# Optimization experiments

Hardware: AMD Instinct MI355X
Metric: run time of the kernel (lower is better)

## Reference

```python
import jax, jax.numpy as jnp
import numpy as np

N = 50000
D = 128
E = 600000


def setup_inputs() -> dict:
    key = jax.random.key(0)
    k1, k2, k3, k4, k5, k6 = jax.random.split(key, 6)
    x = jax.random.normal(k1, (N, D), dtype=jnp.float32)
    edge_index = jax.random.randint(k2, (2, E), 0, N, dtype=jnp.int32)
    s = 1.0 / np.sqrt(D)
    W1 = jax.random.uniform(k3, (D, D), dtype=jnp.float32, minval=-s, maxval=s)
    b1 = jax.random.uniform(k4, (D,), dtype=jnp.float32, minval=-s, maxval=s)
    W2 = jax.random.uniform(k5, (D, D), dtype=jnp.float32, minval=-s, maxval=s)
    b2 = jax.random.uniform(k6, (D,), dtype=jnp.float32, minval=-s, maxval=s)
    return {"x": x, "edge_index": edge_index, "W1": W1, "b1": b1, "W2": W2, "b2": b2}


def _gcn_conv(x, src, dst, W, b):
    # PyG GCNConv (default flow source->target): out[dst] += norm * (x @ W)[src] + b
    n = x.shape[0]
    deg = jax.ops.segment_sum(jnp.ones_like(dst, dtype=x.dtype), dst, num_segments=n)
    dinv = jnp.where(deg > 0, jax.lax.rsqrt(deg), 0.0)
    norm = dinv[src] * dinv[dst]          # [E+N]
    h = x @ W                             # [N, D]
    msg = h[src] * norm[:, None]          # [E+N, D] gather + scale
    out = jax.ops.segment_sum(msg, dst, num_segments=n)
    return out + b


def reference(x, edge_index, W1, b1, W2, b2):
    n = x.shape[0]
    loops = jnp.arange(n, dtype=edge_index.dtype)
    src = jnp.concatenate([edge_index[0], loops])  # add self-loops
    dst = jnp.concatenate([edge_index[1], loops])
    h = jax.nn.relu(_gcn_conv(x, src, dst, W1, b1))
    out = jax.nn.relu(_gcn_conv(h, src, dst, W2, b2))
    return out
```

## Files before the change

### kernel.cpp

```cpp
#include <hip/hip_runtime.h>
#include <stdint.h>

typedef __attribute__((ext_vector_type(8))) short bf16x8;
typedef __attribute__((ext_vector_type(4))) float f32x4;

#define CAP 64
#define SEGCAP 4096

__device__ __forceinline__ float bf2f(unsigned int u) {
    union { unsigned int i; float f; } v; v.i = u << 16; return v.f;
}
__device__ __forceinline__ unsigned int f2bf(float f) {
    union { float f; unsigned int i; } v; v.f = f;
    unsigned int b = v.i;
    b += 0x7FFFu + ((b >> 16) & 1u);
    return b >> 16;
}


__global__ __launch_bounds__(256) void partition_kernel(
    const int* __restrict__ src, const int* __restrict__ dst, int E,
    unsigned int* __restrict__ gcnt,
    unsigned int* __restrict__ seg,
    const float* __restrict__ W1, const float* __restrict__ W2,
    unsigned short* __restrict__ Wt1, unsigned short* __restrict__ Wt2)
{
    __shared__ unsigned int hist[256];
    int tid = threadIdx.x;
    int t = blockIdx.x * 256 + tid;

    if (t < 32768) {
        const float* W = (t < 16384) ? W1 : W2;
        unsigned short* O = (t < 16384) ? Wt1 : Wt2;
        int i = t & 16383;
        O[i] = (unsigned short)f2bf(W[(i & 127) * 128 + (i >> 7)]);
    }

    hist[tid] = 0;
    __syncthreads();

    int e0 = blockIdx.x * 2048 + tid * 8;
    unsigned int pair[8]; int rng[8]; bool val[8];
    if (e0 + 8 <= E) {
        int4 a0 = *(const int4*)(src + e0), a1 = *(const int4*)(src + e0 + 4);
        int4 b0 = *(const int4*)(dst + e0), b1 = *(const int4*)(dst + e0 + 4);
        int sa[8] = {a0.x,a0.y,a0.z,a0.w,a1.x,a1.y,a1.z,a1.w};
        int da[8] = {b0.x,b0.y,b0.z,b0.w,b1.x,b1.y,b1.z,b1.w};
#pragma unroll
        for (int u = 0; u < 8; ++u) {
            pair[u] = ((unsigned int)da[u] << 16) | (unsigned int)sa[u];
            rng[u] = da[u] >> 8; val[u] = true;
        }
    } else {
#pragma unroll
        for (int u = 0; u < 8; ++u) {
            int e = e0 + u;
            val[u] = (e < E);
            int s = val[u] ? src[e] : 0, d = val[u] ? dst[e] : 0;
            pair[u] = ((unsigned int)d << 16) | (unsigned int)s;
            rng[u] = d >> 8;
        }
    }

#pragma unroll
    for (int u = 0; u < 8; ++u)
        if (val[u]) atomicAdd(&hist[rng[u]], 1u);
    __syncthreads();

    {
        unsigned int c = hist[tid];
        if (c) hist[tid] = atomicAdd(&gcnt[tid], c);
    }
    __syncthreads();

#pragma unroll
    for (int u = 0; u < 8; ++u)
        if (val[u]) {
            unsigned int pos = atomicAdd(&hist[rng[u]], 1u);
            if (pos < SEGCAP) seg[(size_t)rng[u] * SEGCAP + pos] = pair[u];
        }
}


__global__ __launch_bounds__(256) void bucket_build(
    const unsigned int* __restrict__ gcnt,
    const unsigned int* __restrict__ seg,
    int* __restrict__ counts, unsigned short* __restrict__ bucket, int N)
{
    __shared__ unsigned int cnt[256];
    int r = blockIdx.x, tid = threadIdx.x;
    cnt[tid] = 0;
    __syncthreads();

    int er = min((int)gcnt[r], SEGCAP);
    const unsigned int* s = seg + (size_t)r * SEGCAP;
#pragma unroll 1
    for (int i = tid; i < er; i += 256) {
        unsigned int pr = s[i];
        int d = pr >> 16;
        int slot = (int)atomicAdd(&cnt[d & 255], 1u);
        if (slot < CAP - 1)
            bucket[(size_t)d * CAP + slot + 1] = (unsigned short)(pr & 0xFFFFu);
    }
    __syncthreads();

    int n = r * 256 + tid;
    if (n < N) {
        int deg = (int)cnt[tid];
        counts[n] = deg;
        bucket[(size_t)n * CAP] = (unsigned short)n;
        int rows = 1 + min(deg, CAP - 1);
        int pe = (rows + 15) & ~15;
        for (int idx = rows; idx < pe; ++idx)
            bucket[(size_t)n * CAP + idx] = (unsigned short)N;
    }
}


__global__ __launch_bounds__(256) void gemm128(const float* __restrict__ A,
                                               const unsigned short* __restrict__ Wt,
                                               const int* __restrict__ counts,
                                               unsigned short* __restrict__ G, int M) {
    int t = threadIdx.x;
    int wave = t >> 6, lane = t & 63;
    int mrow = lane & 15, quad = lane >> 4;

    if (blockIdx.x == 0 && t < 64)
        ((unsigned int*)G)[(size_t)M * 64 + t] = 0u;

    int m0 = (blockIdx.x * 4 + wave) * 16;
    int arow = m0 + mrow;
    int srow = arow < M ? arow : M - 1;
    const float* Arow = A + (size_t)srow * 128;

    f32x4 acc[8];
#pragma unroll
    for (int nt = 0; nt < 8; ++nt) acc[nt] = (f32x4){0.f, 0.f, 0.f, 0.f};

#pragma unroll
    for (int kb = 0; kb < 4; ++kb) {
        f32x4 lo = *(const f32x4*)(Arow + kb * 32 + quad * 8);
        f32x4 hi = *(const f32x4*)(Arow + kb * 32 + quad * 8 + 4);
        bf16x8 a;
#pragma unroll
        for (int i = 0; i < 4; ++i) { a[i] = (short)f2bf(lo[i]); a[i + 4] = (short)f2bf(hi[i]); }
#pragma unroll
        for (int nt = 0; nt < 8; ++nt) {
            bf16x8 b = *(const bf16x8*)(Wt + (size_t)(nt * 16 + mrow) * 128 + kb * 32 + quad * 8);
            acc[nt] = __builtin_amdgcn_mfma_f32_16x16x32_bf16(a, b, acc[nt], 0, 0, 0);
        }
    }

#pragma unroll
    for (int r = 0; r < 4; ++r) {
        int row = m0 + quad * 4 + r;
        if (row < M) {
            float dr = rsqrtf((float)counts[row] + 1.0f);
#pragma unroll
            for (int nt = 0; nt < 8; ++nt)
                G[(size_t)row * 128 + nt * 16 + mrow] = (unsigned short)f2bf(acc[nt][r] * dr);
        }
    }
}


template <bool FINAL>
__global__ __launch_bounds__(256) void agg_kernel(const unsigned short* __restrict__ g,
                                                  const int* __restrict__ counts,
                                                  const unsigned short* __restrict__ bucket,
                                                  const float* __restrict__ bias,
                                                  const unsigned short* __restrict__ Wt,
                                                  unsigned short* __restrict__ G2,
                                                  float* __restrict__ outf,
                                                  int N) {
    __shared__ __align__(16) unsigned short As[FINAL ? 1 : 16][136];
    int wave = threadIdx.x >> 6, lane = threadIdx.x & 63;
    int p = lane & 15, grp = lane >> 4;
    const char* gb = (const char*)g;
    int nb0 = blockIdx.x * 16 + wave * 4;

    if (!FINAL && blockIdx.x == 0 && threadIdx.x < 64)
        ((unsigned int*)G2)[(size_t)N * 64 + threadIdx.x] = 0u;

    float4 bva = ((const float4*)bias)[p * 2];
    float4 bvb = ((const float4*)bias)[p * 2 + 1];

    int degs[4]; unsigned int svs[4];
#pragma unroll
    for (int i = 0; i < 4; ++i) {
        int n = min(nb0 + i, N - 1);
        degs[i] = counts[n];
        svs[i]  = bucket[(size_t)n * CAP + lane];
    }

    uint4 vq[4][4];
#pragma unroll
    for (int i = 0; i < 4; ++i)
#pragma unroll
        for (int q = 0; q < 4; ++q) {
            int s = __shfl((int)svs[i], 4 * q + grp);
            vq[i][q] = *(const uint4*)(gb + (size_t)s * 256 + p * 16);
        }

#pragma unroll
    for (int i = 0; i < 4; ++i) {
        int deg = degs[i];
        int rows = 1 + min(deg, CAP - 1);
        int mr = (rows + 15) & ~15;
        float di = rsqrtf((float)deg + 1.0f);
        float acc[8];
#pragma unroll
        for (int k = 0; k < 8; ++k) acc[k] = 0.f;
#pragma unroll
        for (int q = 0; q < 4; ++q)
#pragma unroll
            for (int d = 0; d < 4; ++d) {
                unsigned int v = (&vq[i][q].x)[d];
                acc[d * 2]     += bf2f(v & 0xFFFFu);
                acc[d * 2 + 1] += bf2f(v >> 16);
            }
#pragma unroll 1
        for (int j0 = 16; j0 < mr; j0 += 16) {
            uint4 tq[4];
#pragma unroll
            for (int q = 0; q < 4; ++q) {
                int s = __shfl((int)svs[i], j0 + 4 * q + grp);
                tq[q] = *(const uint4*)(gb + (size_t)s * 256 + p * 16);
            }
#pragma unroll
            for (int q = 0; q < 4; ++q)
#pragma unroll
                for (int d = 0; d < 4; ++d) {
                    unsigned int v = (&tq[q].x)[d];
                    acc[d * 2]     += bf2f(v & 0xFFFFu);
                    acc[d * 2 + 1] += bf2f(v >> 16);
                }
        }
#pragma unroll
        for (int k = 0; k < 8; ++k) {
            acc[k] += __shfl_xor(acc[k], 16);
            acc[k] += __shfl_xor(acc[k], 32);
        }
        float o[8];
        o[0] = fmaxf(acc[0] * di + bva.x, 0.f);
        o[1] = fmaxf(acc[1] * di + bva.y, 0.f);
        o[2] = fmaxf(acc[2] * di + bva.z, 0.f);
        o[3] = fmaxf(acc[3] * di + bva.w, 0.f);
        o[4] = fmaxf(acc[4] * di + bvb.x, 0.f);
        o[5] = fmaxf(acc[5] * di + bvb.y, 0.f);
        o[6] = fmaxf(acc[6] * di + bvb.z, 0.f);
        o[7] = fmaxf(acc[7] * di + bvb.w, 0.f);

        if (FINAL) {
            if (grp == i) {
                int n = nb0 + i;
                if (n < N) {
                    float4* op = (float4*)(outf + (size_t)n * 128 + p * 8);
                    op[0] = make_float4(o[0], o[1], o[2], o[3]);
                    op[1] = make_float4(o[4], o[5], o[6], o[7]);
                }
            }
        } else {
            if (grp == i) {
                uint4 w;
                w.x = f2bf(o[0]) | (f2bf(o[1]) << 16);
                w.y = f2bf(o[2]) | (f2bf(o[3]) << 16);
                w.z = f2bf(o[4]) | (f2bf(o[5]) << 16);
                w.w = f2bf(o[6]) | (f2bf(o[7]) << 16);
                *(uint4*)&As[wave * 4 + i][p * 8] = w;
            }
        }
    }

    if (FINAL) return;

    __syncthreads();

    int mrow = lane & 15, quad = lane >> 4;
    f32x4 acc2[2];
    acc2[0] = (f32x4){0.f, 0.f, 0.f, 0.f};
    acc2[1] = (f32x4){0.f, 0.f, 0.f, 0.f};
#pragma unroll
    for (int kb = 0; kb < 4; ++kb) {
        bf16x8 a = *(const bf16x8*)(&As[mrow][kb * 32 + quad * 8]);
#pragma unroll
        for (int q = 0; q < 2; ++q) {
            int nt = wave * 2 + q;
            bf16x8 b = *(const bf16x8*)(Wt + (size_t)(nt * 16 + mrow) * 128 + kb * 32 + quad * 8);
            acc2[q] = __builtin_amdgcn_mfma_f32_16x16x32_bf16(a, b, acc2[q], 0, 0, 0);
        }
    }
#pragma unroll
    for (int r = 0; r < 4; ++r) {
        int row = blockIdx.x * 16 + quad * 4 + r;
        if (row < N) {
            float dr = rsqrtf((float)counts[row] + 1.0f);
#pragma unroll
            for (int q = 0; q < 2; ++q) {
                int nt = wave * 2 + q;
                G2[(size_t)row * 128 + nt * 16 + mrow] = (unsigned short)f2bf(acc2[q][r] * dr);
            }
        }
    }
}


extern "C" void kernel_launch(void* const* d_in, const int* in_sizes, int n_in,
                              void* d_out, int out_size, void* d_ws, size_t ws_size,
                              hipStream_t stream) {
    const float* x  = (const float*)d_in[0];
    const int*   ei = (const int*)d_in[1];
    const float* W1 = (const float*)d_in[2];
    const float* b1 = (const float*)d_in[3];
    const float* W2 = (const float*)d_in[4];
    const float* b2 = (const float*)d_in[5];
    float* out = (float*)d_out;

    int N = in_sizes[0] / 128;
    int E = in_sizes[1] / 2;
    const int* src = ei;
    const int* dst = ei + E;
    int NR = (N + 255) >> 8;

    char* p = (char*)d_ws;
    auto alloc = [&](size_t bytes) {
        char* r = p; p += (bytes + 255) & ~(size_t)255; return r;
    };
    int*            counts = (int*)           alloc((size_t)N * 4);
    unsigned short* bucket = (unsigned short*)alloc((size_t)N * CAP * 2);
    unsigned short* g1     = (unsigned short*)alloc((size_t)(N + 1) * 128 * 2);
    unsigned short* g2     = (unsigned short*)alloc((size_t)(N + 1) * 128 * 2);
    unsigned short* Wt1    = (unsigned short*)alloc(16384 * 2);
    unsigned short* Wt2    = (unsigned short*)alloc(16384 * 2);
    unsigned int*   gcnt   = (unsigned int*)  alloc(256 * 4);
    unsigned int*   seg    = (unsigned int*)  alloc((size_t)256 * SEGCAP * 4);

    hipMemsetAsync(gcnt, 0, 256 * 4, stream);

    int ablk = (E + 2047) / 2048;
    if (ablk < 128) ablk = 128;
    partition_kernel<<<ablk, 256, 0, stream>>>(src, dst, E, gcnt, seg, W1, W2, Wt1, Wt2);
    bucket_build<<<NR, 256, 0, stream>>>(gcnt, seg, counts, bucket, N);

    gemm128<<<(N + 63) / 64, 256, 0, stream>>>(x, Wt1, counts, g1, N);
    agg_kernel<false><<<(N + 15) / 16, 256, 0, stream>>>(g1, counts, bucket, b1, Wt2, g2, nullptr, N);
    agg_kernel<true ><<<(N + 15) / 16, 256, 0, stream>>>(g2, counts, bucket, b2, nullptr, nullptr, out, N);
}
```

Measured before the change: 179.8 us.

## Split feature dim into 4 column slabs for gather locality; unfuse second GEMM

Stores the transformed features in a column-sliced layout (4 slabs of 32 bf16 columns per node) so each aggregation pass gathers only 64-byte rows from a smaller working set that fits the cache better. Aggregation runs as 4 passes over the node tiles, one per slab, and the layer-2 GEMM is moved out of the aggregation kernel into a separate gemm launch that reads the slabbed bf16 hidden state. This trades an extra kernel launch and an extra write and read of the hidden activations for better cache reuse during the random-index gathers. It also repeats the bucket and count reads once per pass.

```diff
diff --git a/kernel.cpp b/kernel.cpp
--- a/kernel.cpp
+++ b/kernel.cpp
@@ -117,7 +117,8 @@
 }
 
 
-__global__ __launch_bounds__(256) void gemm128(const float* __restrict__ A,
+template <bool BF16IN>
+__global__ __launch_bounds__(256) void gemm128(const void* __restrict__ Ain,
                                                const unsigned short* __restrict__ Wt,
                                                const int* __restrict__ counts,
                                                unsigned short* __restrict__ G, int M) {
@@ -125,13 +126,14 @@
     int wave = t >> 6, lane = t & 63;
     int mrow = lane & 15, quad = lane >> 4;
 
-    if (blockIdx.x == 0 && t < 64)
-        ((unsigned int*)G)[(size_t)M * 64 + t] = 0u;
+    if (blockIdx.x == 0 && t < 64) {
+        int s = t >> 4, w = t & 15;
+        ((unsigned int*)G)[((size_t)s * (M + 1) + M) * 16 + w] = 0u;
+    }
 
     int m0 = (blockIdx.x * 4 + wave) * 16;
     int arow = m0 + mrow;
     int srow = arow < M ? arow : M - 1;
-    const float* Arow = A + (size_t)srow * 128;
 
     f32x4 acc[8];
 #pragma unroll
@@ -139,11 +141,17 @@
 
 #pragma unroll
     for (int kb = 0; kb < 4; ++kb) {
-        f32x4 lo = *(const f32x4*)(Arow + kb * 32 + quad * 8);
-        f32x4 hi = *(const f32x4*)(Arow + kb * 32 + quad * 8 + 4);
         bf16x8 a;
-#pragma unroll
-        for (int i = 0; i < 4; ++i) { a[i] = (short)f2bf(lo[i]); a[i + 4] = (short)f2bf(hi[i]); }
+        if (BF16IN) {
+            const unsigned short* H = (const unsigned short*)Ain;
+            a = *(const bf16x8*)(H + ((size_t)kb * (M + 1) + srow) * 32 + quad * 8);
+        } else {
+            const float* Arow = (const float*)Ain + (size_t)srow * 128;
+            f32x4 lo = *(const f32x4*)(Arow + kb * 32 + quad * 8);
+            f32x4 hi = *(const f32x4*)(Arow + kb * 32 + quad * 8 + 4);
+#pragma unroll
+            for (int i = 0; i < 4; ++i) { a[i] = (short)f2bf(lo[i]); a[i + 4] = (short)f2bf(hi[i]); }
+        }
 #pragma unroll
         for (int nt = 0; nt < 8; ++nt) {
             bf16x8 b = *(const bf16x8*)(Wt + (size_t)(nt * 16 + mrow) * 128 + kb * 32 + quad * 8);
@@ -157,33 +165,33 @@
         if (row < M) {
             float dr = rsqrtf((float)counts[row] + 1.0f);
 #pragma unroll
-            for (int nt = 0; nt < 8; ++nt)
-                G[(size_t)row * 128 + nt * 16 + mrow] = (unsigned short)f2bf(acc[nt][r] * dr);
+            for (int nt = 0; nt < 8; ++nt) {
+                int c = nt * 16 + mrow;
+                G[((size_t)(c >> 5) * (M + 1) + row) * 32 + (c & 31)] =
+                    (unsigned short)f2bf(acc[nt][r] * dr);
+            }
         }
     }
 }
 
 
 template <bool FINAL>
-__global__ __launch_bounds__(256) void agg_kernel(const unsigned short* __restrict__ g,
-                                                  const int* __restrict__ counts,
-                                                  const unsigned short* __restrict__ bucket,
-                                                  const float* __restrict__ bias,
-                                                  const unsigned short* __restrict__ Wt,
-                                                  unsigned short* __restrict__ G2,
-                                                  float* __restrict__ outf,
-                                                  int N) {
-    __shared__ __align__(16) unsigned short As[FINAL ? 1 : 16][136];
+__global__ __launch_bounds__(256) void aggpass(const unsigned short* __restrict__ g,
+                                               const int* __restrict__ counts,
+                                               const unsigned short* __restrict__ bucket,
+                                               const float* __restrict__ bias,
+                                               unsigned short* __restrict__ H,
+                                               float* __restrict__ outf,
+                                               int N) {
     int wave = threadIdx.x >> 6, lane = threadIdx.x & 63;
-    int p = lane & 15, grp = lane >> 4;
-    const char* gb = (const char*)g;
-    int nb0 = blockIdx.x * 16 + wave * 4;
-
-    if (!FINAL && blockIdx.x == 0 && threadIdx.x < 64)
-        ((unsigned int*)G2)[(size_t)N * 64 + threadIdx.x] = 0u;
-
-    float4 bva = ((const float4*)bias)[p * 2];
-    float4 bvb = ((const float4*)bias)[p * 2 + 1];
+    int p16 = lane & 15, grp = lane >> 4;
+    int NT = gridDim.x >> 2;
+    int pass = blockIdx.x / NT;
+    int tile = blockIdx.x - pass * NT;
+    int nb0 = tile * 16 + wave * 4;
+
+    const unsigned int* gs = (const unsigned int*)g + (size_t)pass * (N + 1) * 16;
+    float2 bv = ((const float2*)bias)[pass * 16 + p16];
 
     int degs[4]; unsigned int svs[4];
 #pragma unroll
@@ -193,13 +201,13 @@
         svs[i]  = bucket[(size_t)n * CAP + lane];
     }
 
-    uint4 vq[4][4];
+    unsigned int vv[4][4];
 #pragma unroll
     for (int i = 0; i < 4; ++i)
 #pragma unroll
         for (int q = 0; q < 4; ++q) {
             int s = __shfl((int)svs[i], 4 * q + grp);
-            vq[i][q] = *(const uint4*)(gb + (size_t)s * 256 + p * 16);
+            vv[i][q] = gs[(size_t)s * 16 + p16];
         }
 
 #pragma unroll
@@ -208,97 +216,42 @@
         int rows = 1 + min(deg, CAP - 1);
         int mr = (rows + 15) & ~15;
         float di = rsqrtf((float)deg + 1.0f);
-        float acc[8];
-#pragma unroll
-        for (int k = 0; k < 8; ++k) acc[k] = 0.f;
-#pragma unroll
-        for (int q = 0; q < 4; ++q)
-#pragma unroll
-            for (int d = 0; d < 4; ++d) {
-                unsigned int v = (&vq[i][q].x)[d];
-                acc[d * 2]     += bf2f(v & 0xFFFFu);
-                acc[d * 2 + 1] += bf2f(v >> 16);
-            }
+        float a0 = 0.f, a1 = 0.f;
+#pragma unroll
+        for (int q = 0; q < 4; ++q) {
+            unsigned int v = vv[i][q];
+            a0 += bf2f(v & 0xFFFFu);
+            a1 += bf2f(v >> 16);
+        }
 #pragma unroll 1
         for (int j0 = 16; j0 < mr; j0 += 16) {
-            uint4 tq[4];
+            unsigned int tq[4];
 #pragma unroll
             for (int q = 0; q < 4; ++q) {
                 int s = __shfl((int)svs[i], j0 + 4 * q + grp);
-                tq[q] = *(const uint4*)(gb + (size_t)s * 256 + p * 16);
+                tq[q] = gs[(size_t)s * 16 + p16];
             }
 #pragma unroll
-            for (int q = 0; q < 4; ++q)
-#pragma unroll
-                for (int d = 0; d < 4; ++d) {
-                    unsigned int v = (&tq[q].x)[d];
-                    acc[d * 2]     += bf2f(v & 0xFFFFu);
-                    acc[d * 2 + 1] += bf2f(v >> 16);
+            for (int q = 0; q < 4; ++q) {
+                unsigned int v = tq[q];
+                a0 += bf2f(v & 0xFFFFu);
+                a1 += bf2f(v >> 16);
+            }
+        }
+        a0 += __shfl_xor(a0, 16); a0 += __shfl_xor(a0, 32);
+        a1 += __shfl_xor(a1, 16); a1 += __shfl_xor(a1, 32);
+        float o0 = fmaxf(a0 * di + bv.x, 0.f);
+        float o1 = fmaxf(a1 * di + bv.y, 0.f);
+
+        if (grp == i) {
+            int n = nb0 + i;
+            if (n < N) {
+                if (FINAL) {
+                    ((float2*)(outf + (size_t)n * 128 + pass * 32))[p16] = make_float2(o0, o1);
+                } else {
+                    ((unsigned int*)H)[((size_t)pass * (N + 1) + n) * 16 + p16] =
+                        f2bf(o0) | (f2bf(o1) << 16);
                 }
-        }
-#pragma unroll
-        for (int k = 0; k < 8; ++k) {
-            acc[k] += __shfl_xor(acc[k], 16);
-            acc[k] += __shfl_xor(acc[k], 32);
-        }
-        float o[8];
-        o[0] = fmaxf(acc[0] * di + bva.x, 0.f);
-        o[1] = fmaxf(acc[1] * di + bva.y, 0.f);
-        o[2] = fmaxf(acc[2] * di + bva.z, 0.f);
-        o[3] = fmaxf(acc[3] * di + bva.w, 0.f);
-        o[4] = fmaxf(acc[4] * di + bvb.x, 0.f);
-        o[5] = fmaxf(acc[5] * di + bvb.y, 0.f);
-        o[6] = fmaxf(acc[6] * di + bvb.z, 0.f);
-        o[7] = fmaxf(acc[7] * di + bvb.w, 0.f);
-
-        if (FINAL) {
-            if (grp == i) {
-                int n = nb0 + i;
-                if (n < N) {
-                    float4* op = (float4*)(outf + (size_t)n * 128 + p * 8);
-                    op[0] = make_float4(o[0], o[1], o[2], o[3]);
-                    op[1] = make_float4(o[4], o[5], o[6], o[7]);
-                }
-            }
-        } else {
-            if (grp == i) {
-                uint4 w;
-                w.x = f2bf(o[0]) | (f2bf(o[1]) << 16);
-                w.y = f2bf(o[2]) | (f2bf(o[3]) << 16);
-                w.z = f2bf(o[4]) | (f2bf(o[5]) << 16);
-                w.w = f2bf(o[6]) | (f2bf(o[7]) << 16);
-                *(uint4*)&As[wave * 4 + i][p * 8] = w;
-            }
-        }
-    }
-
-    if (FINAL) return;
-
-    __syncthreads();
-
-    int mrow = lane & 15, quad = lane >> 4;
-    f32x4 acc2[2];
-    acc2[0] = (f32x4){0.f, 0.f, 0.f, 0.f};
-    acc2[1] = (f32x4){0.f, 0.f, 0.f, 0.f};
-#pragma unroll
-    for (int kb = 0; kb < 4; ++kb) {
-        bf16x8 a = *(const bf16x8*)(&As[mrow][kb * 32 + quad * 8]);
-#pragma unroll
-        for (int q = 0; q < 2; ++q) {
-            int nt = wave * 2 + q;
-            bf16x8 b = *(const bf16x8*)(Wt + (size_t)(nt * 16 + mrow) * 128 + kb * 32 + quad * 8);
-            acc2[q] = __builtin_amdgcn_mfma_f32_16x16x32_bf16(a, b, acc2[q], 0, 0, 0);
-        }
-    }
-#pragma unroll
-    for (int r = 0; r < 4; ++r) {
-        int row = blockIdx.x * 16 + quad * 4 + r;
-        if (row < N) {
-            float dr = rsqrtf((float)counts[row] + 1.0f);
-#pragma unroll
-            for (int q = 0; q < 2; ++q) {
-                int nt = wave * 2 + q;
-                G2[(size_t)row * 128 + nt * 16 + mrow] = (unsigned short)f2bf(acc2[q][r] * dr);
             }
         }
     }
@@ -330,6 +283,7 @@
     unsigned short* bucket = (unsigned short*)alloc((size_t)N * CAP * 2);
     unsigned short* g1     = (unsigned short*)alloc((size_t)(N + 1) * 128 * 2);
     unsigned short* g2     = (unsigned short*)alloc((size_t)(N + 1) * 128 * 2);
+    unsigned short* h1     = (unsigned short*)alloc((size_t)(N + 1) * 128 * 2);
     unsigned short* Wt1    = (unsigned short*)alloc(16384 * 2);
     unsigned short* Wt2    = (unsigned short*)alloc(16384 * 2);
     unsigned int*   gcnt   = (unsigned int*)  alloc(256 * 4);
@@ -339,10 +293,13 @@
 
     int ablk = (E + 2047) / 2048;
     if (ablk < 128) ablk = 128;
+    int NT = (N + 15) / 16;
+
     partition_kernel<<<ablk, 256, 0, stream>>>(src, dst, E, gcnt, seg, W1, W2, Wt1, Wt2);
     bucket_build<<<NR, 256, 0, stream>>>(gcnt, seg, counts, bucket, N);
 
-    gemm128<<<(N + 63) / 64, 256, 0, stream>>>(x, Wt1, counts, g1, N);
-    agg_kernel<false><<<(N + 15) / 16, 256, 0, stream>>>(g1, counts, bucket, b1, Wt2, g2, nullptr, N);
-    agg_kernel<true ><<<(N + 15) / 16, 256, 0, stream>>>(g2, counts, bucket, b2, nullptr, nullptr, out, N);
-}
+    gemm128<false><<<(N + 63) / 64, 256, 0, stream>>>(x,  Wt1, counts, g1, N);
+    aggpass<false><<<4 * NT, 256, 0, stream>>>(g1, counts, bucket, b1, h1, nullptr, N);
+    gemm128<true ><<<(N + 63) / 64, 256, 0, stream>>>(h1, Wt2, counts, g2, N);
+    aggpass<true ><<<4 * NT, 256, 0, stream>>>(g2, counts, bucket, b2, nullptr, out, N);
+}
```

Result: slower. 198.6 us (+10.4%).
